# Performance work log

Measured on AMD Instinct MI355X. Metric: run time of the kernel, lower is better.

Reference implementation:

```python
import jax, jax.numpy as jnp
import numpy as np

NPOINT = 512
RADIUS = 0.2
NSAMPLE = 32
BN_EPS = 1e-5


def setup_inputs() -> dict:
    key = jax.random.key(0)
    ks = jax.random.split(key, 8)
    B, N, C = 8, 16384, 64
    xyz = jax.random.uniform(ks[0], (B, N, 3), dtype=jnp.float32)
    features = jax.random.normal(ks[1], (B, N, C), dtype=jnp.float32)
    # shared-MLP 1x1 conv weights (out, in), BN params per layer
    w0 = jax.random.normal(ks[2], (64, 67), dtype=jnp.float32) * 0.1
    w1 = jax.random.normal(ks[3], (64, 64), dtype=jnp.float32) * 0.1
    w2 = jax.random.normal(ks[4], (128, 64), dtype=jnp.float32) * 0.1
    return dict(
        xyz=xyz, features=features,
        w0=w0, g0=jnp.ones((64,)), b0=jnp.zeros((64,)), m0=jnp.zeros((64,)), v0=jnp.ones((64,)),
        w1=w1, g1=jnp.ones((64,)), b1=jnp.zeros((64,)), m1=jnp.zeros((64,)), v1=jnp.ones((64,)),
        w2=w2, g2=jnp.ones((128,)), b2=jnp.zeros((128,)), m2=jnp.zeros((128,)), v2=jnp.ones((128,)),
    )


def furthest_point_sample(xyz, npoint):
    # xyz: (B, N, 3) -> idx: (B, npoint) int32. Sequential farthest-point selection.
    B, N, _ = xyz.shape
    binds = jnp.arange(B)

    def step(carry, _):
        dists, last = carry  # (B,N), (B,)
        p = xyz[binds, last]                      # (B, 3)
        d = jnp.sum((xyz - p[:, None, :]) ** 2, axis=-1)  # (B, N)
        dists = jnp.minimum(dists, d)
        nxt = jnp.argmax(dists, axis=-1).astype(jnp.int32)
        return (dists, nxt), last

    init = (jnp.full((B, N), jnp.inf, dtype=xyz.dtype), jnp.zeros((B,), jnp.int32))
    _, idx = jax.lax.scan(step, init, None, length=npoint)  # (npoint, B)
    return idx.T  # (B, npoint)


def ball_query(xyz, new_xyz, radius, nsample):
    # xyz: (B,N,3), new_xyz: (B,S,3) -> idx (B,S,nsample) int32
    N = xyz.shape[1]
    d2 = jnp.sum((new_xyz[:, :, None, :] - xyz[:, None, :, :]) ** 2, axis=-1)  # (B,S,N)
    cand = jnp.where(d2 <= radius * radius, jnp.arange(N, dtype=jnp.int32), N)
    cand = jnp.sort(cand, axis=-1)[..., :nsample]  # first nsample in-radius indices
    first = cand[..., :1]
    idx = jnp.where(cand == N, first, cand)       # duplicate first hit when short
    return jnp.minimum(idx, N - 1)


def _mlp_layer(x, w, g, b, m, v):
    # x: (B,S,K,Cin); 1x1 conv + BN(inference) + ReLU
    h = jnp.einsum('bskc,oc->bsko', x, w)
    h = (h - m) * (g * jax.lax.rsqrt(v + BN_EPS)) + b
    return jax.nn.relu(h)


def reference(xyz, features, w0, g0, b0, m0, v0, w1, g1, b1, m1, v1, w2, g2, b2, m2, v2):
    B = xyz.shape[0]
    binds = jnp.arange(B)[:, None, None]
    fps_idx = furthest_point_sample(xyz, NPOINT)                # (B, S)
    new_xyz = jnp.take_along_axis(xyz, fps_idx[..., None], axis=1)  # (B, S, 3)
    idx = ball_query(xyz, new_xyz, RADIUS, NSAMPLE)             # (B, S, K)
    grouped_xyz = xyz[binds, idx] - new_xyz[:, :, None, :]      # (B,S,K,3) centered
    grouped_feat = features[binds, idx]                         # (B,S,K,C)
    x = jnp.concatenate([grouped_xyz, grouped_feat], axis=-1)   # (B,S,K,3+C)
    x = _mlp_layer(x, w0, g0, b0, m0, v0)
    x = _mlp_layer(x, w1, g1, b1, m1, v1)
    x = _mlp_layer(x, w2, g2, b2, m2, v2)                       # (B,S,K,128)
    new_features = jnp.max(x, axis=2)                           # max-pool over nsample
    new_features = jnp.transpose(new_features, (0, 2, 1))       # (B, 128, S) channel-first
    return new_xyz, new_features
```

## Files before the change

kernel.cpp:

```cpp
#include <hip/hip_runtime.h>
#include <hip/hip_bf16.h>

#define NPT   16384
#define NQ    512
#define NS    32
#define BATCH 8

typedef float f32x2 __attribute__((ext_vector_type(2)));

__device__ inline f32x2 pk_add(f32x2 a, f32x2 b)
{
    f32x2 d;
    asm("v_pk_add_f32 %0, %1, %2" : "=v"(d) : "v"(a), "v"(b));
    return d;
}
__device__ inline f32x2 pk_mul(f32x2 a, f32x2 b)
{
    f32x2 d;
    asm("v_pk_mul_f32 %0, %1, %2" : "=v"(d) : "v"(a), "v"(b));
    return d;
}

template <int CTRL>
__device__ inline double dpp_f64(double x)
{
    const unsigned long long u = (unsigned long long)__double_as_longlong(x);
    int lo = (int)(unsigned)u;
    int hi = (int)(unsigned)(u >> 32);
    lo = __builtin_amdgcn_update_dpp(0, lo, CTRL, 0xf, 0xf, true);
    hi = __builtin_amdgcn_update_dpp(0, hi, CTRL, 0xf, 0xf, true);
    return __longlong_as_double(
        (long long)(((unsigned long long)(unsigned)hi << 32) | (unsigned)lo));
}

__global__ __launch_bounds__(512)
__attribute__((amdgpu_waves_per_eu(2, 2)))
void fps_kernel(const float* __restrict__ xyz, float* __restrict__ new_xyz)
{
#pragma clang fp contract(off)
    const int b = blockIdx.x;
    const int t = threadIdx.x;
    const float* xb = xyz + (size_t)b * NPT * 3;

    f32x2 xr[16], yr[16], zr[16], dr[16];
    const float INF = __int_as_float(0x7f800000);
#pragma unroll
    for (int j = 0; j < 16; ++j) {
        const int p0 = (2 * j) * 512 + t;
        const int p1 = (2 * j + 1) * 512 + t;
        xr[j] = (f32x2){xb[p0 * 3 + 0], xb[p1 * 3 + 0]};
        yr[j] = (f32x2){xb[p0 * 3 + 1], xb[p1 * 3 + 1]};
        zr[j] = (f32x2){xb[p0 * 3 + 2], xb[p1 * 3 + 2]};
        dr[j] = (f32x2){INF, INF};
    }

    __shared__ unsigned long long red[2][8];

    float px = xb[0], py = xb[1], pz = xb[2];

    for (int s = 0; s < NQ; ++s) {
        if (t == 0) {
            float* o = new_xyz + ((size_t)b * NQ + s) * 3;
            o[0] = px; o[1] = py; o[2] = pz;
        }
        if (s == NQ - 1) break;

        const float nx = -px, ny = -py, nz = -pz;
        const f32x2 npx = {nx, nx}, npy = {ny, ny}, npz = {nz, nz};
        float dmax = -1.0f;
        int   bi_  = 0;
#pragma unroll
        for (int j = 0; j < 16; ++j) {
            const f32x2 dx = pk_add(xr[j], npx);
            const f32x2 dy = pk_add(yr[j], npy);
            const f32x2 dz = pk_add(zr[j], npz);
            f32x2 d = pk_add(pk_mul(dx, dx), pk_mul(dy, dy));
            d = pk_add(d, pk_mul(dz, dz));
            f32x2 dn;
            dn.x = fminf(dr[j].x, d.x);
            dn.y = fminf(dr[j].y, d.y);
            dr[j] = dn;
            const float ds = fmaxf(dn.x, dn.y);
            const int   is = (dn.x >= dn.y) ? (2 * j) : (2 * j + 1);
            if (ds > dmax) { dmax = ds; bi_ = is; }
        }

        const unsigned pidx = (unsigned)(bi_ * 512 + t);
        double kd = __longlong_as_double((long long)(
            ((unsigned long long)__float_as_uint(dmax) << 32) | (unsigned)(~pidx)));

        kd = fmax(kd, dpp_f64<0x111>(kd));
        kd = fmax(kd, dpp_f64<0x112>(kd));
        kd = fmax(kd, dpp_f64<0x114>(kd));
        kd = fmax(kd, dpp_f64<0x118>(kd));
        kd = fmax(kd, dpp_f64<0x142>(kd));
        kd = fmax(kd, dpp_f64<0x143>(kd));

        if ((t & 63) == 63)
            red[s & 1][t >> 6] = (unsigned long long)__double_as_longlong(kd);
        __syncthreads();

        double kc = __longlong_as_double((long long)red[s & 1][t & 7]);
        kc = fmax(kc, dpp_f64<0x111>(kc));
        kc = fmax(kc, dpp_f64<0x112>(kc));
        kc = fmax(kc, dpp_f64<0x114>(kc));

        const unsigned long long kw = (unsigned long long)__double_as_longlong(kc);
        const unsigned lo7 = (unsigned)__builtin_amdgcn_readlane((int)(unsigned)kw, 7);
        const int nxt = (int)(unsigned)(~lo7);

        px = xb[nxt * 3 + 0];
        py = xb[nxt * 3 + 1];
        pz = xb[nxt * 3 + 2];
    }
}

__global__ __launch_bounds__(256) void bq_kernel(const float* __restrict__ xyz,
                                                 const float* __restrict__ newxyz,
                                                 int* __restrict__ gidx)
{
    const int wid  = (blockIdx.x * 256 + threadIdx.x) >> 6;
    const int lane = threadIdx.x & 63;
    const int b    = wid >> 9;
    const float* xb = xyz + (size_t)b * NPT * 3;

    const float qx = newxyz[wid * 3 + 0];
    const float qy = newxyz[wid * 3 + 1];
    const float qz = newxyz[wid * 3 + 2];
    int* out = gidx + (size_t)wid * NS;

    const float R2 = 0.04f;
    int cnt = 0, first = -1;

    for (int base = 0; base < NPT; base += 64) {
        const int p = base + lane;
        const float dx = __fsub_rn(xb[p * 3 + 0], qx);
        const float dy = __fsub_rn(xb[p * 3 + 1], qy);
        const float dz = __fsub_rn(xb[p * 3 + 2], qz);
        const float d  = __fadd_rn(__fadd_rn(__fmul_rn(dx, dx), __fmul_rn(dy, dy)),
                                   __fmul_rn(dz, dz));
        const bool in = (d <= R2);
        const unsigned long long m = __ballot(in);
        if (first < 0 && m) first = base + (__ffsll((unsigned long long)m) - 1);
        if (in) {
            const int pos = cnt + __popcll(m & ((1ull << lane) - 1ull));
            if (pos < NS) out[pos] = p;
        }
        cnt += __popcll(m);
        if (cnt >= NS) break;
    }
    if (cnt < NS) {
        const int f = (cnt > 0) ? first : (NPT - 1);
        for (int j = cnt + lane; j < NS; j += 64) out[j] = f;
    }
}

template <int OP>
__device__ inline void mlp_layer(const float* __restrict__ inb,
                                 const float* __restrict__ wbuf,
                                 const float* __restrict__ scp,
                                 const float* __restrict__ bip,
                                 float* __restrict__ outb, int nchunk, int t)
{
    const int ko = t & 15;
    const int og = t >> 4;
    const int o0 = og * OP;
    float acc0[OP], acc1[OP];
#pragma unroll
    for (int j = 0; j < OP; ++j) { acc0[j] = 0.f; acc1[j] = 0.f; }

    for (int cc = 0; cc < nchunk; ++cc) {
        const int c = cc * 4;
        const float4 xa = *(const float4*)(inb + ko * 68 + c);
        const float4 xb = *(const float4*)(inb + (ko + 16) * 68 + c);
#pragma unroll
        for (int j = 0; j < OP; ++j) {
            const float4 w = *(const float4*)(wbuf + (o0 + j) * 68 + c);
            acc0[j] += xa.x * w.x + xa.y * w.y + xa.z * w.z + xa.w * w.w;
            acc1[j] += xb.x * w.x + xb.y * w.y + xb.z * w.z + xb.w * w.w;
        }
    }
#pragma unroll
    for (int j = 0; j < OP; ++j) {
        const float sv = scp[o0 + j], bv = bip[o0 + j];
        acc0[j] = fmaxf(acc0[j] * sv + bv, 0.f);
        acc1[j] = fmaxf(acc1[j] * sv + bv, 0.f);
    }
#pragma unroll
    for (int jb = 0; jb < OP; jb += 4) {
        *(float4*)(outb + ko * 68 + o0 + jb) =
            make_float4(acc0[jb], acc0[jb + 1], acc0[jb + 2], acc0[jb + 3]);
        *(float4*)(outb + (ko + 16) * 68 + o0 + jb) =
            make_float4(acc1[jb], acc1[jb + 1], acc1[jb + 2], acc1[jb + 3]);
    }
}

__device__ inline void mlp_layer2(const float* __restrict__ inb,
                                  const float* __restrict__ wbuf,
                                  const float* __restrict__ scp,
                                  const float* __restrict__ bip,
                                  float* __restrict__ out, int b, int s, int t)
{
    const int ko = t & 15;
    const int og = t >> 4;
    const int o0 = og * 8;
    float acc0[8], acc1[8];
#pragma unroll
    for (int j = 0; j < 8; ++j) { acc0[j] = 0.f; acc1[j] = 0.f; }

    for (int cc = 0; cc < 16; ++cc) {
        const int c = cc * 4;
        const float4 xa = *(const float4*)(inb + ko * 68 + c);
        const float4 xb = *(const float4*)(inb + (ko + 16) * 68 + c);
#pragma unroll
        for (int j = 0; j < 8; ++j) {
            const float4 w = *(const float4*)(wbuf + (o0 + j) * 68 + c);
            acc0[j] += xa.x * w.x + xa.y * w.y + xa.z * w.z + xa.w * w.w;
            acc1[j] += xb.x * w.x + xb.y * w.y + xb.z * w.z + xb.w * w.w;
        }
    }
    float v[8];
#pragma unroll
    for (int j = 0; j < 8; ++j) {
        const float sv = scp[o0 + j], bv = bip[o0 + j];
        const float h0 = fmaxf(acc0[j] * sv + bv, 0.f);
        const float h1 = fmaxf(acc1[j] * sv + bv, 0.f);
        v[j] = fmaxf(h0, h1);
    }
#pragma unroll
    for (int m = 1; m <= 8; m <<= 1) {
#pragma unroll
        for (int j = 0; j < 8; ++j) v[j] = fmaxf(v[j], __shfl_xor(v[j], m, 64));
    }
    if (ko == 0) {
#pragma unroll
        for (int j = 0; j < 8; ++j)
            out[((size_t)b * 128 + o0 + j) * NQ + s] = v[j];
    }
}

__global__ __launch_bounds__(256) void mlp_kernel(
    const float* __restrict__ xyz, const float* __restrict__ feat,
    const float* __restrict__ newxyz, const int* __restrict__ gidx,
    const float* __restrict__ w0, const float* __restrict__ g0,
    const float* __restrict__ b0, const float* __restrict__ m0,
    const float* __restrict__ v0,
    const float* __restrict__ w1, const float* __restrict__ g1,
    const float* __restrict__ b1, const float* __restrict__ m1,
    const float* __restrict__ v1,
    const float* __restrict__ w2, const float* __restrict__ g2,
    const float* __restrict__ b2, const float* __restrict__ m2,
    const float* __restrict__ v2,
    float* __restrict__ out)
{
    __shared__ float wbuf[128 * 68];
    __shared__ float bufA[32 * 68];
    __shared__ float bufB[32 * 68];
    __shared__ float sc[256], bi[256];

    const int t   = threadIdx.x;
    const int grp = blockIdx.x;
    const int b   = grp >> 9;
    const int s   = grp & (NQ - 1);
    const int* gi = gidx + (size_t)grp * NS;

    if (t < 64) {
        const float sv = g0[t] * rsqrtf(v0[t] + 1e-5f);
        sc[t] = sv; bi[t] = b0[t] - m0[t] * sv;
    } else if (t < 128) {
        const int j = t - 64;
        const float sv = g1[j] * rsqrtf(v1[j] + 1e-5f);
        sc[t] = sv; bi[t] = b1[j] - m1[j] * sv;
    } else {
        const int j = t - 128;
        const float sv = g2[j] * rsqrtf(v2[j] + 1e-5f);
        sc[t] = sv; bi[t] = b2[j] - m2[j] * sv;
    }

    for (int i = t; i < 64 * 68; i += 256) {
        const int o = i / 68, c = i - o * 68;
        float v;
        if (c < 64)       v = w0[o * 67 + 3 + c];
        else if (c < 67)  v = w0[o * 67 + (c - 64)];
        else              v = 0.f;
        wbuf[i] = v;
    }

    {
        const int k = t >> 3, f = t & 7;
        const int p = gi[k];
        const float* fr = feat + ((size_t)b * NPT + p) * 64 + f * 8;
        const float4 a0 = *(const float4*)fr;
        const float4 a1 = *(const float4*)(fr + 4);
        *(float4*)(bufA + k * 68 + f * 8)     = a0;
        *(float4*)(bufA + k * 68 + f * 8 + 4) = a1;
        if (f == 0) {
            const float qx = newxyz[grp * 3 + 0];
            const float qy = newxyz[grp * 3 + 1];
            const float qz = newxyz[grp * 3 + 2];
            const float* xp = xyz + ((size_t)b * NPT + p) * 3;
            bufA[k * 68 + 64] = xp[0] - qx;
            bufA[k * 68 + 65] = xp[1] - qy;
            bufA[k * 68 + 66] = xp[2] - qz;
            bufA[k * 68 + 67] = 0.f;
        }
    }
    __syncthreads();

    mlp_layer<4>(bufA, wbuf, sc, bi, bufB, 17, t);
    __syncthreads();

    for (int i = t; i < 64 * 68; i += 256) {
        const int o = i / 68, c = i - o * 68;
        wbuf[i] = (c < 64) ? w1[o * 64 + c] : 0.f;
    }
    __syncthreads();

    mlp_layer<4>(bufB, wbuf, sc + 64, bi + 64, bufA, 16, t);
    __syncthreads();

    for (int i = t; i < 128 * 68; i += 256) {
        const int o = i / 68, c = i - o * 68;
        wbuf[i] = (c < 64) ? w2[o * 64 + c] : 0.f;
    }
    __syncthreads();

    mlp_layer2(bufA, wbuf, sc + 128, bi + 128, out, b, s, t);
}

extern "C" void kernel_launch(void* const* d_in, const int* in_sizes, int n_in,
                              void* d_out, int out_size, void* d_ws, size_t ws_size,
                              hipStream_t stream)
{
    const float* xyz  = (const float*)d_in[0];
    const float* feat = (const float*)d_in[1];
    const float* w0 = (const float*)d_in[2];
    const float* g0 = (const float*)d_in[3];
    const float* b0 = (const float*)d_in[4];
    const float* m0 = (const float*)d_in[5];
    const float* v0 = (const float*)d_in[6];
    const float* w1 = (const float*)d_in[7];
    const float* g1 = (const float*)d_in[8];
    const float* b1 = (const float*)d_in[9];
    const float* m1 = (const float*)d_in[10];
    const float* v1 = (const float*)d_in[11];
    const float* w2 = (const float*)d_in[12];
    const float* g2 = (const float*)d_in[13];
    const float* b2 = (const float*)d_in[14];
    const float* m2 = (const float*)d_in[15];
    const float* v2 = (const float*)d_in[16];

    float* out      = (float*)d_out;
    float* new_xyz  = out;
    float* out_feat = out + BATCH * NQ * 3;
    int*   gidx     = (int*)d_ws;

    fps_kernel<<<BATCH, 512, 0, stream>>>(xyz, new_xyz);
    bq_kernel<<<(BATCH * NQ * 64) / 256, 256, 0, stream>>>(xyz, new_xyz, gidx);
    mlp_kernel<<<BATCH * NQ, 256, 0, stream>>>(xyz, feat, new_xyz, gidx,
                                               w0, g0, b0, m0, v0,
                                               w1, g1, b1, m1, v1,
                                               w2, g2, b2, m2, v2,
                                               out_feat);
}
```

Before: 1.197 ms.

## Split FPS across eight blocks per batch with global atomic reduction

Farthest point sampling now splits each batch's 16384 points across 8 workgroups of 256 threads instead of one workgroup of 512. Each block reduces its local argmax and combines it through a global atomic max, with an arrival counter it spins on every iteration. A memset clears the sync area before launch. This spreads the distance update over more CUs, but adds a device-scope atomic round trip and a spin barrier on each of the 511 sequential steps. It also relies on all 64 blocks being resident at once to avoid deadlock.

```diff
diff --git a/kernel.cpp b/kernel.cpp
--- a/kernel.cpp
+++ b/kernel.cpp
@@ -1,10 +1,13 @@
 #include <hip/hip_runtime.h>
 #include <hip/hip_bf16.h>
 
-#define NPT   16384
-#define NQ    512
-#define NS    32
-#define BATCH 8
+#define NPT     16384
+#define NQ      512
+#define NS      32
+#define BATCH   8
+#define CHUNKS  8
+#define FPS_TPB 256
+#define CPTS    (NPT / CHUNKS)
 
 typedef float f32x2 __attribute__((ext_vector_type(2)));
 
@@ -33,33 +36,40 @@
         (long long)(((unsigned long long)(unsigned)hi << 32) | (unsigned)lo));
 }
 
-__global__ __launch_bounds__(512)
-__attribute__((amdgpu_waves_per_eu(2, 2)))
-void fps_kernel(const float* __restrict__ xyz, float* __restrict__ new_xyz)
+__global__ __launch_bounds__(FPS_TPB, 1)
+void fps_kernel(const float* __restrict__ xyz, float* __restrict__ new_xyz,
+                unsigned long long* __restrict__ gkey, unsigned* __restrict__ gcnt)
 {
 #pragma clang fp contract(off)
-    const int b = blockIdx.x;
-    const int t = threadIdx.x;
+    const int blk = blockIdx.x;
+    const int b   = blk >> 3;
+    const int c   = blk & 7;
+    const int t   = threadIdx.x;
     const float* xb = xyz + (size_t)b * NPT * 3;
-
-    f32x2 xr[16], yr[16], zr[16], dr[16];
+    const int base = c * CPTS;
+
+    f32x2 xr[4], yr[4], zr[4], dr[4];
     const float INF = __int_as_float(0x7f800000);
 #pragma unroll
-    for (int j = 0; j < 16; ++j) {
-        const int p0 = (2 * j) * 512 + t;
-        const int p1 = (2 * j + 1) * 512 + t;
+    for (int j = 0; j < 4; ++j) {
+        const int p0 = base + (2 * j) * FPS_TPB + t;
+        const int p1 = base + (2 * j + 1) * FPS_TPB + t;
         xr[j] = (f32x2){xb[p0 * 3 + 0], xb[p1 * 3 + 0]};
         yr[j] = (f32x2){xb[p0 * 3 + 1], xb[p1 * 3 + 1]};
         zr[j] = (f32x2){xb[p0 * 3 + 2], xb[p1 * 3 + 2]};
         dr[j] = (f32x2){INF, INF};
     }
 
-    __shared__ unsigned long long red[2][8];
+    __shared__ unsigned long long red[4];
+    __shared__ unsigned long long bc;
+
+    unsigned long long* gk = gkey + (size_t)b * NQ;
+    unsigned*           gc = gcnt + (size_t)b * NQ;
 
     float px = xb[0], py = xb[1], pz = xb[2];
 
     for (int s = 0; s < NQ; ++s) {
-        if (t == 0) {
+        if (c == 0 && t == 0) {
             float* o = new_xyz + ((size_t)b * NQ + s) * 3;
             o[0] = px; o[1] = py; o[2] = pz;
         }
@@ -70,7 +80,7 @@
         float dmax = -1.0f;
         int   bi_  = 0;
 #pragma unroll
-        for (int j = 0; j < 16; ++j) {
+        for (int j = 0; j < 4; ++j) {
             const f32x2 dx = pk_add(xr[j], npx);
             const f32x2 dy = pk_add(yr[j], npy);
             const f32x2 dz = pk_add(zr[j], npz);
@@ -85,7 +95,7 @@
             if (ds > dmax) { dmax = ds; bi_ = is; }
         }
 
-        const unsigned pidx = (unsigned)(bi_ * 512 + t);
+        const unsigned pidx = (unsigned)(base + bi_ * FPS_TPB + t);
         double kd = __longlong_as_double((long long)(
             ((unsigned long long)__float_as_uint(dmax) << 32) | (unsigned)(~pidx)));
 
@@ -97,21 +107,24 @@
         kd = fmax(kd, dpp_f64<0x143>(kd));
 
         if ((t & 63) == 63)
-            red[s & 1][t >> 6] = (unsigned long long)__double_as_longlong(kd);
+            red[t >> 6] = (unsigned long long)__double_as_longlong(kd);
         __syncthreads();
 
-        double kc = __longlong_as_double((long long)red[s & 1][t & 7]);
-        kc = fmax(kc, dpp_f64<0x111>(kc));
-        kc = fmax(kc, dpp_f64<0x112>(kc));
-        kc = fmax(kc, dpp_f64<0x114>(kc));
-
-        const unsigned long long kw = (unsigned long long)__double_as_longlong(kc);
-        const unsigned lo7 = (unsigned)__builtin_amdgcn_readlane((int)(unsigned)kw, 7);
-        const int nxt = (int)(unsigned)(~lo7);
-
+        if (t == 0) {
+            unsigned long long kb = red[0];
+            for (int w = 1; w < 4; ++w) { const unsigned long long o = red[w]; if (o > kb) kb = o; }
+            __hip_atomic_fetch_max(&gk[s], kb, __ATOMIC_RELAXED, __HIP_MEMORY_SCOPE_AGENT);
+            __hip_atomic_fetch_add(&gc[s], 1u, __ATOMIC_ACQ_REL, __HIP_MEMORY_SCOPE_AGENT);
+            while (__hip_atomic_load(&gc[s], __ATOMIC_ACQUIRE, __HIP_MEMORY_SCOPE_AGENT) < CHUNKS) { }
+            bc = __hip_atomic_load(&gk[s], __ATOMIC_ACQUIRE, __HIP_MEMORY_SCOPE_AGENT);
+        }
+        __syncthreads();
+
+        const int nxt = (int)(unsigned)(~(unsigned)bc);
         px = xb[nxt * 3 + 0];
         py = xb[nxt * 3 + 1];
         pz = xb[nxt * 3 + 2];
+        __syncthreads();
     }
 }
 
@@ -353,9 +366,15 @@
     float* out      = (float*)d_out;
     float* new_xyz  = out;
     float* out_feat = out + BATCH * NQ * 3;
-    int*   gidx     = (int*)d_ws;
-
-    fps_kernel<<<BATCH, 512, 0, stream>>>(xyz, new_xyz);
+
+    int*   gidx = (int*)d_ws;
+    char*  syncbase = (char*)d_ws + 4096 * NS * sizeof(int);
+    unsigned long long* gkey = (unsigned long long*)syncbase;
+    unsigned* gcnt = (unsigned*)(syncbase + BATCH * NQ * 8);
+
+    hipMemsetAsync(syncbase, 0, BATCH * NQ * 12, stream);
+
+    fps_kernel<<<BATCH * CHUNKS, FPS_TPB, 0, stream>>>(xyz, new_xyz, gkey, gcnt);
     bq_kernel<<<(BATCH * NQ * 64) / 256, 256, 0, stream>>>(xyz, new_xyz, gidx);
     mlp_kernel<<<BATCH * NQ, 256, 0, stream>>>(xyz, feat, new_xyz, gidx,
                                                w0, g0, b0, m0, v0,
```

Result: slower. 1.608 ms (+34.4%).
